# Performance work log

Hardware: AMD Instinct MI355X
Metric: run time of the kernel (lower is better)

## Reference

```python
import jax, jax.numpy as jnp
import numpy as np

ROUTING_ITERS = 3

def squash(t, axis=-1):
    sq_norm = jnp.sum(t * t, axis=axis, keepdims=True)
    scale = sq_norm / (1.0 + sq_norm)
    return scale * t / jnp.sqrt(sq_norm + 1e-8)

def setup_inputs() -> dict:
    key = jax.random.key(0)
    k1, k2 = jax.random.split(key)
    B, N, I, J, O = 64, 2048, 16, 32, 32
    x = jax.random.normal(k1, (B, N, I), dtype=jnp.float32)
    weights = jax.random.normal(k2, (N, J, O, I), dtype=jnp.float32) * 0.1
    return {"x": x, "weights": weights}

def reference(x, weights):
    B, N, _ = x.shape
    J = weights.shape[1]
    # predictions u_{j|i}: [B, N, J, O]
    predictions = jnp.einsum('bni,njoi->bnjo', x, weights)
    b = jnp.zeros((B, N, J, 1), dtype=x.dtype)
    v = None
    for i in range(ROUTING_ITERS):
        c = jax.nn.softmax(b, axis=2)                      # coupling over capsules J
        s = jnp.sum(predictions * c, axis=1, keepdims=True)  # [B,1,J,O]
        v = squash(s, axis=-1)
        if i < ROUTING_ITERS - 1:
            agreement = jnp.sum(predictions * v, axis=-1, keepdims=True)  # [B,N,J,1]
            b = b + agreement
    return jnp.squeeze(v, axis=1)  # [B, J, O]
```

## Files before the change

kernel.cpp:

```cpp
#include <hip/hip_runtime.h>
#include <hip/hip_bf16.h>

#define B_ 64
#define N_ 2048
#define I_ 16
#define J_ 32
#define O_ 32
#define JO_ 1024
#define WSPLITS 32
#define SFSPLITS 64

typedef __attribute__((ext_vector_type(8))) short bf16x8;
typedef __attribute__((ext_vector_type(16))) float f32x16;
typedef unsigned short u16;
typedef unsigned int u32;

__device__ __forceinline__ float bf2f(u16 u) {
  union { u32 i; float f; } c; c.i = ((u32)u) << 16; return c.f;
}
__device__ __forceinline__ u16 f2bf(float f) {
  union { float f; u32 i; } c; c.f = f;
  u32 r = (c.i + 0x7fffu + ((c.i >> 16) & 1u)) >> 16;
  return (u16)r;
}
__device__ __forceinline__ u32 pack2_pk(float lo, float hi) {
  u32 r;
  asm("v_cvt_pk_bf16_f32 %0, %1, %2" : "=v"(r) : "v"(lo), "v"(hi));
  return r;
}
__device__ __forceinline__ u32 scale2_pk(u32 p, float cv) {
  union { u32 i; float f; } lo, hi;
  lo.i = p << 16; hi.i = p & 0xffff0000u;
  return pack2_pk(lo.f * cv, hi.f * cv);
}
__device__ __forceinline__ float dot16(const f32x16& p, uint4 lo, uint4 hi) {
  const u32 w[8] = {lo.x, lo.y, lo.z, lo.w, hi.x, hi.y, hi.z, hi.w};
  float s = 0.f;
  #pragma unroll
  for (int k = 0; k < 8; ++k) {
    union { u32 i; float f; } a, b;
    a.i = w[k] << 16; b.i = w[k] & 0xffff0000u;
    s += p[2 * k] * a.f + p[2 * k + 1] * b.f;
  }
  return s;
}

__global__ __launch_bounds__(256) void xconv_kernel(
    const float* __restrict__ xf, u16* __restrict__ xt)
{
  const int idx = blockIdx.x * 256 + threadIdx.x;
  const int b = idx >> 11, n = idx & 2047;
  const float4* sp = (const float4*)(xf + (size_t)idx * 16);
  float4 f0 = sp[0], f1 = sp[1], f2 = sp[2], f3 = sp[3];
  uint4 d0, d1;
  d0.x = pack2_pk(f0.x, f0.y); d0.y = pack2_pk(f0.z, f0.w);
  d0.z = pack2_pk(f1.x, f1.y); d0.w = pack2_pk(f1.z, f1.w);
  d1.x = pack2_pk(f2.x, f2.y); d1.y = pack2_pk(f2.z, f2.w);
  d1.z = pack2_pk(f3.x, f3.y); d1.w = pack2_pk(f3.z, f3.w);
  uint4* dp = (uint4*)(xt + ((size_t)n * 64 + b) * 16);
  dp[0] = d0; dp[1] = d1;
}

#define WSF_NPW 16

__global__ __launch_bounds__(256, 4) void wsf_kernel(
    const float* __restrict__ wf, u16* __restrict__ wb,
    const u16* __restrict__ xt, float* __restrict__ s_part)
{
  __shared__ float red[4][2048];
  const int tid = threadIdx.x;
  const int wave = tid >> 6, lane = tid & 63;
  const int l31 = lane & 31, h = lane >> 5;
  const int j = blockIdx.x, split = blockIdx.y;
  const int n0 = (split * 4 + wave) * WSF_NPW;
  f32x16 acc0 = {0.f, 0.f, 0.f, 0.f, 0.f, 0.f, 0.f, 0.f,
                 0.f, 0.f, 0.f, 0.f, 0.f, 0.f, 0.f, 0.f};
  f32x16 acc1 = acc0;

  #pragma unroll 4
  for (int i = 0; i < WSF_NPW; ++i) {
    const int n = n0 + i;
    const size_t row = (size_t)n * JO_ + j * 32 + l31;
    const float* wsrc = wf + row * 16 + h * 8;
    const float4 f0 = *(const float4*)(wsrc);
    const float4 f1 = *(const float4*)(wsrc + 4);
    union { uint4 u4; bf16x8 bv; } wd;
    wd.u4.x = pack2_pk(f0.x, f0.y); wd.u4.y = pack2_pk(f0.z, f0.w);
    wd.u4.z = pack2_pk(f1.x, f1.y); wd.u4.w = pack2_pk(f1.z, f1.w);
    *(uint4*)(wb + row * 16 + h * 8) = wd.u4;
    const bf16x8 x0 = *(const bf16x8*)(xt + ((size_t)n * 64 + l31) * 16 + h * 8);
    const bf16x8 x1 = *(const bf16x8*)(xt + ((size_t)n * 64 + 32 + l31) * 16 + h * 8);
    acc0 = __builtin_amdgcn_mfma_f32_32x32x16_bf16(wd.bv, x0, acc0, 0, 0, 0);
    acc1 = __builtin_amdgcn_mfma_f32_32x32x16_bf16(wd.bv, x1, acc1, 0, 0, 0);
  }
  #pragma unroll
  for (int r = 0; r < 16; ++r) {
    const int o = (r & 3) + 8 * (r >> 2) + 4 * h;
    red[wave][o * 64 + l31] = acc0[r];
    red[wave][o * 64 + 32 + l31] = acc1[r];
  }
  __syncthreads();
  float* dst = s_part + (size_t)split * (JO_ * B_) + (size_t)j * 32 * 64;
  #pragma unroll
  for (int k = 0; k < 8; ++k) {
    const int idx = tid + 256 * k;
    dst[idx] = red[0][idx] + red[1][idx] + red[2][idx] + red[3][idx];
  }
}

#define SF_NPW 8

__global__ __launch_bounds__(256, 4) void sf_kernel(
    const u16* __restrict__ xt, const u16* __restrict__ wb,
    const u16* __restrict__ ct, float* __restrict__ s_part)
{
  __shared__ float red[4][2048];
  const int tid = threadIdx.x;
  const int wave = tid >> 6, lane = tid & 63;
  const int l31 = lane & 31, h = lane >> 5;
  const int j = blockIdx.x, split = blockIdx.y;
  const int n0 = (split * 4 + wave) * SF_NPW;
  f32x16 acc0 = {0.f, 0.f, 0.f, 0.f, 0.f, 0.f, 0.f, 0.f,
                 0.f, 0.f, 0.f, 0.f, 0.f, 0.f, 0.f, 0.f};
  f32x16 acc1 = acc0;

  bf16x8 wfr = *(const bf16x8*)(wb + ((size_t)n0 * JO_ + j * 32 + l31) * 16 + h * 8);
  union { bf16x8 v; u32 u[4]; } xa, xb;
  xa.v = *(const bf16x8*)(xt + ((size_t)n0 * 64 + l31) * 16 + h * 8);
  xb.v = *(const bf16x8*)(xt + ((size_t)n0 * 64 + 32 + l31) * 16 + h * 8);
  float cv0 = bf2f(ct[((size_t)j * N_ + n0) * 64 + l31]);
  float cv1 = bf2f(ct[((size_t)j * N_ + n0) * 64 + 32 + l31]);

  #pragma unroll 1
  for (int i = 0; i < SF_NPW; ++i) {
    bf16x8 wfr_n = wfr;
    union { bf16x8 v; u32 u[4]; } xa_n, xb_n;
    xa_n.v = xa.v; xb_n.v = xb.v;
    float c0n = cv0, c1n = cv1;
    if (i + 1 < SF_NPW) {
      const int n1 = n0 + i + 1;
      wfr_n = *(const bf16x8*)(wb + ((size_t)n1 * JO_ + j * 32 + l31) * 16 + h * 8);
      xa_n.v = *(const bf16x8*)(xt + ((size_t)n1 * 64 + l31) * 16 + h * 8);
      xb_n.v = *(const bf16x8*)(xt + ((size_t)n1 * 64 + 32 + l31) * 16 + h * 8);
      c0n = bf2f(ct[((size_t)j * N_ + n1) * 64 + l31]);
      c1n = bf2f(ct[((size_t)j * N_ + n1) * 64 + 32 + l31]);
    }
    union { bf16x8 v; u32 u[4]; } s0, s1;
    s0.u[0] = scale2_pk(xa.u[0], cv0); s0.u[1] = scale2_pk(xa.u[1], cv0);
    s0.u[2] = scale2_pk(xa.u[2], cv0); s0.u[3] = scale2_pk(xa.u[3], cv0);
    s1.u[0] = scale2_pk(xb.u[0], cv1); s1.u[1] = scale2_pk(xb.u[1], cv1);
    s1.u[2] = scale2_pk(xb.u[2], cv1); s1.u[3] = scale2_pk(xb.u[3], cv1);
    acc0 = __builtin_amdgcn_mfma_f32_32x32x16_bf16(wfr, s0.v, acc0, 0, 0, 0);
    acc1 = __builtin_amdgcn_mfma_f32_32x32x16_bf16(wfr, s1.v, acc1, 0, 0, 0);
    wfr = wfr_n; xa.v = xa_n.v; xb.v = xb_n.v; cv0 = c0n; cv1 = c1n;
  }
  #pragma unroll
  for (int r = 0; r < 16; ++r) {
    const int o = (r & 3) + 8 * (r >> 2) + 4 * h;
    red[wave][o * 64 + l31] = acc0[r];
    red[wave][o * 64 + 32 + l31] = acc1[r];
  }
  __syncthreads();
  float* dst = s_part + (size_t)split * (JO_ * B_) + (size_t)j * 32 * 64;
  #pragma unroll
  for (int k = 0; k < 8; ++k) {
    const int idx = tid + 256 * k;
    dst[idx] = red[0][idx] + red[1][idx] + red[2][idx] + red[3][idx];
  }
}

__global__ __launch_bounds__(256) void rs_kernel(
    const float* __restrict__ src, float* __restrict__ dst, int nsplit)
{
  const int idx = blockIdx.x * 256 + threadIdx.x;
  float s = 0.f;
  #pragma unroll 8
  for (int p = 0; p < nsplit; ++p) s += src[(size_t)p * (JO_ * B_) + idx];
  dst[idx] = s;
}

__global__ __launch_bounds__(64) void r_kernel(
    const float* __restrict__ s_red, float* __restrict__ v,
    const float* __restrict__ vprev, u16* __restrict__ v4,
    float* __restrict__ out, int mode, float scale)
{
  const int tid = threadIdx.x;
  const int jj = tid >> 5, o = tid & 31;
  const int b = blockIdx.x >> 4, jg = blockIdx.x & 15;
  const int j = jg * 2 + jj;
  const float s = s_red[(size_t)(j * 32 + o) * 64 + b] * scale;
  float sq = s * s;
  #pragma unroll
  for (int m = 16; m >= 1; m >>= 1) sq += __shfl_xor(sq, m, 64);
  const float sc = sq / (1.f + sq) * rsqrtf(sq + 1e-8f);
  const float vv = sc * s;
  const size_t off = (size_t)b * JO_ + j * 32 + o;
  const int g = o >> 3, hh = (o >> 2) & 1, rr = o & 3;
  const size_t v4off = (((size_t)j * 2 + hh) * 64 + b) * 16 + g * 4 + rr;
  if (mode == 0) { v[off] = vv; v4[v4off] = f2bf(vv); }
  else if (mode == 1) { v4[v4off] = f2bf(vv + vprev[off]); }
  else { out[off] = vv; }
}

__global__ __launch_bounds__(256, 4) void a_kernel(
    const u16* __restrict__ xt, const u16* __restrict__ wb,
    const u16* __restrict__ v4, u16* __restrict__ ct)
{
  __shared__ float lgs[64][33];
  const int tid = threadIdx.x;
  const int wave = tid >> 6, lane = tid & 63;
  const int l31 = lane & 31, h = lane >> 5;
  const int n = blockIdx.x;
  const f32x16 zero16 = {0.f, 0.f, 0.f, 0.f, 0.f, 0.f, 0.f, 0.f,
                         0.f, 0.f, 0.f, 0.f, 0.f, 0.f, 0.f, 0.f};

  const bf16x8 x0 = *(const bf16x8*)(xt + ((size_t)n * 64 + l31) * 16 + h * 8);
  const bf16x8 x1 = *(const bf16x8*)(xt + ((size_t)n * 64 + 32 + l31) * 16 + h * 8);

  {
    const int t0 = wave * 8;
    bf16x8 wfr = *(const bf16x8*)(wb + ((size_t)n * JO_ + t0 * 32 + l31) * 16 + h * 8);
    const u16* pa = v4 + (((size_t)t0 * 2 + h) * 64 + l31) * 16;
    const u16* pb = v4 + (((size_t)t0 * 2 + h) * 64 + 32 + l31) * 16;
    uint4 va0 = *(const uint4*)(pa), va1 = *(const uint4*)(pa + 8);
    uint4 vb0 = *(const uint4*)(pb), vb1 = *(const uint4*)(pb + 8);

    #pragma unroll 1
    for (int tt = 0; tt < 8; ++tt) {
      const int t = wave * 8 + tt;
      bf16x8 wfr_n = wfr;
      uint4 va0n = va0, va1n = va1, vb0n = vb0, vb1n = vb1;
      if (tt + 1 < 8) {
        const int t1 = t + 1;
        wfr_n = *(const bf16x8*)(wb + ((size_t)n * JO_ + t1 * 32 + l31) * 16 + h * 8);
        const u16* qa = v4 + (((size_t)t1 * 2 + h) * 64 + l31) * 16;
        const u16* qb = v4 + (((size_t)t1 * 2 + h) * 64 + 32 + l31) * 16;
        va0n = *(const uint4*)(qa); va1n = *(const uint4*)(qa + 8);
        vb0n = *(const uint4*)(qb); vb1n = *(const uint4*)(qb + 8);
      }
      f32x16 p0 = __builtin_amdgcn_mfma_f32_32x32x16_bf16(wfr, x0, zero16, 0, 0, 0);
      f32x16 p1 = __builtin_amdgcn_mfma_f32_32x32x16_bf16(wfr, x1, zero16, 0, 0, 0);
      float s0 = dot16(p0, va0, va1);
      float s1 = dot16(p1, vb0, vb1);
      s0 += __shfl_xor(s0, 32, 64);
      s1 += __shfl_xor(s1, 32, 64);
      lgs[lane][t] = h ? s1 : s0;
      wfr = wfr_n; va0 = va0n; va1 = va1n; vb0 = vb0n; vb1 = vb1n;
    }
  }
  __syncthreads();

  if (tid < 64) {
    const int b = tid;
    float lv[32];
    float mx = -1e30f;
    #pragma unroll
    for (int t = 0; t < 32; ++t) { lv[t] = lgs[b][t]; mx = fmaxf(mx, lv[t]); }
    float sm = 0.f;
    #pragma unroll
    for (int t = 0; t < 32; ++t) { lv[t] = __expf(lv[t] - mx); sm += lv[t]; }
    const float inv = 1.f / sm;
    #pragma unroll
    for (int t = 0; t < 32; ++t) lgs[b][t] = lv[t] * inv;
  }
  __syncthreads();

  #pragma unroll
  for (int k = 0; k < 8; ++k) {
    const int idx = k * 256 + tid;
    const int t = idx >> 6, b = idx & 63;
    ct[((size_t)t * N_ + n) * 64 + b] = f2bf(lgs[b][t]);
  }
}

extern "C" void kernel_launch(void* const* d_in, const int* in_sizes, int n_in,
                              void* d_out, int out_size, void* d_ws, size_t ws_size,
                              hipStream_t stream) {
  const float* x = (const float*)d_in[0];
  const float* w = (const float*)d_in[1];
  float* out = (float*)d_out;
  char* ws = (char*)d_ws;
  u16*   wb       = (u16*)ws;
  u16*   xt       = (u16*)(ws + (size_t)64 * 1024 * 1024);
  float* s_part32 = (float*)(ws + (size_t)68 * 1024 * 1024);
  float* s_red    = (float*)(ws + (size_t)76 * 1024 * 1024);
  float* v0       = (float*)(ws + (size_t)76 * 1024 * 1024 + 262144);
  u16*   v4       = (u16*)(ws + (size_t)76 * 1024 * 1024 + 2 * 262144);
  u16*   ct       = (u16*)(ws + (size_t)78 * 1024 * 1024);
  float* s_partSF = (float*)(ws + (size_t)88 * 1024 * 1024);

  dim3 wsfg(32, WSPLITS), wsfb(256);
  dim3 sfg(32, SFSPLITS), sfb(256);
  dim3 ag(2048), ab(256);
  dim3 rsg(256), rsb(256);
  dim3 rg(1024), rb(64);

  xconv_kernel<<<dim3(512), dim3(256), 0, stream>>>(x, xt);
  wsf_kernel<<<wsfg, wsfb, 0, stream>>>(w, wb, xt, s_part32);
  rs_kernel<<<rsg, rsb, 0, stream>>>(s_part32, s_red, WSPLITS);
  r_kernel<<<rg, rb, 0, stream>>>(s_red, v0, v0, v4, out, 0, 0.03125f);
  a_kernel<<<ag, ab, 0, stream>>>(xt, wb, v4, ct);
  sf_kernel<<<sfg, sfb, 0, stream>>>(xt, wb, ct, s_partSF);
  rs_kernel<<<rsg, rsb, 0, stream>>>(s_partSF, s_red, SFSPLITS);
  r_kernel<<<rg, rb, 0, stream>>>(s_red, v0, v0, v4, out, 1, 1.0f);
  a_kernel<<<ag, ab, 0, stream>>>(xt, wb, v4, ct);
  sf_kernel<<<sfg, sfb, 0, stream>>>(xt, wb, ct, s_partSF);
  rs_kernel<<<rsg, rsb, 0, stream>>>(s_partSF, s_red, SFSPLITS);
  r_kernel<<<rg, rb, 0, stream>>>(s_red, v0, v0, v4, out, 2, 1.0f);
}
```

Baseline: 323.2 us.

## Fuse split reduction and squash into GEMM kernels via atomics and last-block finisher

Replaces the per-split partial buffers plus separate reduce and squash kernels with atomicAdd into a single accumulator. A per-capsule counter lets the last arriving block squash and write v, v4 or the output, and then zero the accumulator for the next pass. It also halves the sf split count while doubling per-wave n work. This drops six kernel launches and the partial-sum traffic, in exchange for atomic contention, nondeterministic float summation order, and a serial tail in the finishing block.

```diff
diff --git a/kernel.cpp b/kernel.cpp
--- a/kernel.cpp
+++ b/kernel.cpp
@@ -8,7 +8,7 @@
 #define O_ 32
 #define JO_ 1024
 #define WSPLITS 32
-#define SFSPLITS 64
+#define SFSPLITS 32
 
 typedef __attribute__((ext_vector_type(8))) short bf16x8;
 typedef __attribute__((ext_vector_type(16))) float f32x16;
@@ -45,8 +45,41 @@
   return s;
 }
 
+__device__ __forceinline__ void squash_finisher(
+    float* __restrict__ s_sum, float* __restrict__ v, u16* __restrict__ v4,
+    float* __restrict__ out, int mode, float scale, int j, int tid,
+    float* fs, float* fsc)
+{
+  #pragma unroll
+  for (int k = 0; k < 8; ++k) {
+    const int idx = tid + 256 * k;
+    fs[idx] = atomicExch(&s_sum[(size_t)j * 2048 + idx], 0.0f) * scale;
+  }
+  __syncthreads();
+  if (tid < 64) {
+    float sq = 0.f;
+    #pragma unroll
+    for (int o = 0; o < 32; ++o) { const float t = fs[o * 64 + tid]; sq += t * t; }
+    fsc[tid] = sq / (1.f + sq) * rsqrtf(sq + 1e-8f);
+  }
+  __syncthreads();
+  #pragma unroll
+  for (int k = 0; k < 8; ++k) {
+    const int idx = tid + 256 * k;
+    const int o = idx >> 6, b = idx & 63;
+    const float vv = fs[idx] * fsc[b];
+    const int g = o >> 3, hh = (o >> 2) & 1, rr = o & 3;
+    const size_t v4off = (((size_t)j * 2 + hh) * 64 + b) * 16 + g * 4 + rr;
+    const size_t off = (size_t)b * JO_ + j * 32 + o;
+    if (mode == 0)      { v[off] = vv; v4[v4off] = f2bf(vv); }
+    else if (mode == 1) { v4[v4off] = f2bf(vv + v[off]); }
+    else                { out[off] = vv; }
+  }
+}
+
 __global__ __launch_bounds__(256) void xconv_kernel(
-    const float* __restrict__ xf, u16* __restrict__ xt)
+    const float* __restrict__ xf, u16* __restrict__ xt,
+    float* __restrict__ s_sum, u32* __restrict__ cnt)
 {
   const int idx = blockIdx.x * 256 + threadIdx.x;
   const int b = idx >> 11, n = idx & 2047;
@@ -59,15 +92,20 @@
   d1.z = pack2_pk(f3.x, f3.y); d1.w = pack2_pk(f3.z, f3.w);
   uint4* dp = (uint4*)(xt + ((size_t)n * 64 + b) * 16);
   dp[0] = d0; dp[1] = d1;
+  if (idx < JO_ * B_) s_sum[idx] = 0.f;
+  if (idx < 96) cnt[idx] = 0;
 }
 
 #define WSF_NPW 16
 
 __global__ __launch_bounds__(256, 4) void wsf_kernel(
     const float* __restrict__ wf, u16* __restrict__ wb,
-    const u16* __restrict__ xt, float* __restrict__ s_part)
+    const u16* __restrict__ xt, float* __restrict__ s_sum,
+    u32* __restrict__ cnt, float* __restrict__ v, u16* __restrict__ v4,
+    float* __restrict__ out)
 {
   __shared__ float red[4][2048];
+  __shared__ u32 isLast;
   const int tid = threadIdx.x;
   const int wave = tid >> 6, lane = tid & 63;
   const int l31 = lane & 31, h = lane >> 5;
@@ -100,21 +138,32 @@
     red[wave][o * 64 + 32 + l31] = acc1[r];
   }
   __syncthreads();
-  float* dst = s_part + (size_t)split * (JO_ * B_) + (size_t)j * 32 * 64;
   #pragma unroll
   for (int k = 0; k < 8; ++k) {
     const int idx = tid + 256 * k;
-    dst[idx] = red[0][idx] + red[1][idx] + red[2][idx] + red[3][idx];
-  }
-}
-
-#define SF_NPW 8
+    const float sum = red[0][idx] + red[1][idx] + red[2][idx] + red[3][idx];
+    atomicAdd(&s_sum[(size_t)j * 2048 + idx], sum);
+  }
+  __syncthreads();
+  if (tid == 0) {
+    __threadfence();
+    isLast = (atomicAdd(&cnt[j], 1u) == WSPLITS - 1);
+  }
+  __syncthreads();
+  if (isLast)
+    squash_finisher(s_sum, v, v4, out, 0, 0.03125f, j, tid, red[0], red[1]);
+}
+
+#define SF_NPW 16
 
 __global__ __launch_bounds__(256, 4) void sf_kernel(
     const u16* __restrict__ xt, const u16* __restrict__ wb,
-    const u16* __restrict__ ct, float* __restrict__ s_part)
+    const u16* __restrict__ ct, float* __restrict__ s_sum,
+    u32* __restrict__ cnt, float* __restrict__ v, u16* __restrict__ v4,
+    float* __restrict__ out, int mode)
 {
   __shared__ float red[4][2048];
+  __shared__ u32 isLast;
   const int tid = threadIdx.x;
   const int wave = tid >> 6, lane = tid & 63;
   const int l31 = lane & 31, h = lane >> 5;
@@ -125,34 +174,34 @@
   f32x16 acc1 = acc0;
 
   bf16x8 wfr = *(const bf16x8*)(wb + ((size_t)n0 * JO_ + j * 32 + l31) * 16 + h * 8);
-  union { bf16x8 v; u32 u[4]; } xa, xb;
-  xa.v = *(const bf16x8*)(xt + ((size_t)n0 * 64 + l31) * 16 + h * 8);
-  xb.v = *(const bf16x8*)(xt + ((size_t)n0 * 64 + 32 + l31) * 16 + h * 8);
+  union { bf16x8 v_; u32 u[4]; } xa, xb;
+  xa.v_ = *(const bf16x8*)(xt + ((size_t)n0 * 64 + l31) * 16 + h * 8);
+  xb.v_ = *(const bf16x8*)(xt + ((size_t)n0 * 64 + 32 + l31) * 16 + h * 8);
   float cv0 = bf2f(ct[((size_t)j * N_ + n0) * 64 + l31]);
   float cv1 = bf2f(ct[((size_t)j * N_ + n0) * 64 + 32 + l31]);
 
   #pragma unroll 1
   for (int i = 0; i < SF_NPW; ++i) {
     bf16x8 wfr_n = wfr;
-    union { bf16x8 v; u32 u[4]; } xa_n, xb_n;
-    xa_n.v = xa.v; xb_n.v = xb.v;
+    union { bf16x8 v_; u32 u[4]; } xa_n, xb_n;
+    xa_n.v_ = xa.v_; xb_n.v_ = xb.v_;
     float c0n = cv0, c1n = cv1;
     if (i + 1 < SF_NPW) {
       const int n1 = n0 + i + 1;
       wfr_n = *(const bf16x8*)(wb + ((size_t)n1 * JO_ + j * 32 + l31) * 16 + h * 8);
-      xa_n.v = *(const bf16x8*)(xt + ((size_t)n1 * 64 + l31) * 16 + h * 8);
-      xb_n.v = *(const bf16x8*)(xt + ((size_t)n1 * 64 + 32 + l31) * 16 + h * 8);
+      xa_n.v_ = *(const bf16x8*)(xt + ((size_t)n1 * 64 + l31) * 16 + h * 8);
+      xb_n.v_ = *(const bf16x8*)(xt + ((size_t)n1 * 64 + 32 + l31) * 16 + h * 8);
       c0n = bf2f(ct[((size_t)j * N_ + n1) * 64 + l31]);
       c1n = bf2f(ct[((size_t)j * N_ + n1) * 64 + 32 + l31]);
     }
-    union { bf16x8 v; u32 u[4]; } s0, s1;
+    union { bf16x8 v_; u32 u[4]; } s0, s1;
     s0.u[0] = scale2_pk(xa.u[0], cv0); s0.u[1] = scale2_pk(xa.u[1], cv0);
     s0.u[2] = scale2_pk(xa.u[2], cv0); s0.u[3] = scale2_pk(xa.u[3], cv0);
     s1.u[0] = scale2_pk(xb.u[0], cv1); s1.u[1] = scale2_pk(xb.u[1], cv1);
     s1.u[2] = scale2_pk(xb.u[2], cv1); s1.u[3] = scale2_pk(xb.u[3], cv1);
-    acc0 = __builtin_amdgcn_mfma_f32_32x32x16_bf16(wfr, s0.v, acc0, 0, 0, 0);
-    acc1 = __builtin_amdgcn_mfma_f32_32x32x16_bf16(wfr, s1.v, acc1, 0, 0, 0);
-    wfr = wfr_n; xa.v = xa_n.v; xb.v = xb_n.v; cv0 = c0n; cv1 = c1n;
+    acc0 = __builtin_amdgcn_mfma_f32_32x32x16_bf16(wfr, s0.v_, acc0, 0, 0, 0);
+    acc1 = __builtin_amdgcn_mfma_f32_32x32x16_bf16(wfr, s1.v_, acc1, 0, 0, 0);
+    wfr = wfr_n; xa.v_ = xa_n.v_; xb.v_ = xb_n.v_; cv0 = c0n; cv1 = c1n;
   }
   #pragma unroll
   for (int r = 0; r < 16; ++r) {
@@ -161,45 +210,20 @@
     red[wave][o * 64 + 32 + l31] = acc1[r];
   }
   __syncthreads();
-  float* dst = s_part + (size_t)split * (JO_ * B_) + (size_t)j * 32 * 64;
   #pragma unroll
   for (int k = 0; k < 8; ++k) {
     const int idx = tid + 256 * k;
-    dst[idx] = red[0][idx] + red[1][idx] + red[2][idx] + red[3][idx];
-  }
-}
-
-__global__ __launch_bounds__(256) void rs_kernel(
-    const float* __restrict__ src, float* __restrict__ dst, int nsplit)
-{
-  const int idx = blockIdx.x * 256 + threadIdx.x;
-  float s = 0.f;
-  #pragma unroll 8
-  for (int p = 0; p < nsplit; ++p) s += src[(size_t)p * (JO_ * B_) + idx];
-  dst[idx] = s;
-}
-
-__global__ __launch_bounds__(64) void r_kernel(
-    const float* __restrict__ s_red, float* __restrict__ v,
-    const float* __restrict__ vprev, u16* __restrict__ v4,
-    float* __restrict__ out, int mode, float scale)
-{
-  const int tid = threadIdx.x;
-  const int jj = tid >> 5, o = tid & 31;
-  const int b = blockIdx.x >> 4, jg = blockIdx.x & 15;
-  const int j = jg * 2 + jj;
-  const float s = s_red[(size_t)(j * 32 + o) * 64 + b] * scale;
-  float sq = s * s;
-  #pragma unroll
-  for (int m = 16; m >= 1; m >>= 1) sq += __shfl_xor(sq, m, 64);
-  const float sc = sq / (1.f + sq) * rsqrtf(sq + 1e-8f);
-  const float vv = sc * s;
-  const size_t off = (size_t)b * JO_ + j * 32 + o;
-  const int g = o >> 3, hh = (o >> 2) & 1, rr = o & 3;
-  const size_t v4off = (((size_t)j * 2 + hh) * 64 + b) * 16 + g * 4 + rr;
-  if (mode == 0) { v[off] = vv; v4[v4off] = f2bf(vv); }
-  else if (mode == 1) { v4[v4off] = f2bf(vv + vprev[off]); }
-  else { out[off] = vv; }
+    const float sum = red[0][idx] + red[1][idx] + red[2][idx] + red[3][idx];
+    atomicAdd(&s_sum[(size_t)j * 2048 + idx], sum);
+  }
+  __syncthreads();
+  if (tid == 0) {
+    __threadfence();
+    isLast = (atomicAdd(&cnt[j], 1u) == SFSPLITS - 1);
+  }
+  __syncthreads();
+  if (isLast)
+    squash_finisher(s_sum, v, v4, out, mode, 1.0f, j, tid, red[0], red[1]);
 }
 
 __global__ __launch_bounds__(256, 4) void a_kernel(
@@ -280,31 +304,21 @@
   const float* w = (const float*)d_in[1];
   float* out = (float*)d_out;
   char* ws = (char*)d_ws;
-  u16*   wb       = (u16*)ws;
-  u16*   xt       = (u16*)(ws + (size_t)64 * 1024 * 1024);
-  float* s_part32 = (float*)(ws + (size_t)68 * 1024 * 1024);
-  float* s_red    = (float*)(ws + (size_t)76 * 1024 * 1024);
-  float* v0       = (float*)(ws + (size_t)76 * 1024 * 1024 + 262144);
-  u16*   v4       = (u16*)(ws + (size_t)76 * 1024 * 1024 + 2 * 262144);
-  u16*   ct       = (u16*)(ws + (size_t)78 * 1024 * 1024);
-  float* s_partSF = (float*)(ws + (size_t)88 * 1024 * 1024);
-
-  dim3 wsfg(32, WSPLITS), wsfb(256);
-  dim3 sfg(32, SFSPLITS), sfb(256);
-  dim3 ag(2048), ab(256);
-  dim3 rsg(256), rsb(256);
-  dim3 rg(1024), rb(64);
-
-  xconv_kernel<<<dim3(512), dim3(256), 0, stream>>>(x, xt);
-  wsf_kernel<<<wsfg, wsfb, 0, stream>>>(w, wb, xt, s_part32);
-  rs_kernel<<<rsg, rsb, 0, stream>>>(s_part32, s_red, WSPLITS);
-  r_kernel<<<rg, rb, 0, stream>>>(s_red, v0, v0, v4, out, 0, 0.03125f);
-  a_kernel<<<ag, ab, 0, stream>>>(xt, wb, v4, ct);
-  sf_kernel<<<sfg, sfb, 0, stream>>>(xt, wb, ct, s_partSF);
-  rs_kernel<<<rsg, rsb, 0, stream>>>(s_partSF, s_red, SFSPLITS);
-  r_kernel<<<rg, rb, 0, stream>>>(s_red, v0, v0, v4, out, 1, 1.0f);
-  a_kernel<<<ag, ab, 0, stream>>>(xt, wb, v4, ct);
-  sf_kernel<<<sfg, sfb, 0, stream>>>(xt, wb, ct, s_partSF);
-  rs_kernel<<<rsg, rsb, 0, stream>>>(s_partSF, s_red, SFSPLITS);
-  r_kernel<<<rg, rb, 0, stream>>>(s_red, v0, v0, v4, out, 2, 1.0f);
-}
+  u16*   wb    = (u16*)ws;
+  u16*   xt    = (u16*)(ws + (size_t)64 * 1024 * 1024);
+  float* s_sum = (float*)(ws + (size_t)68 * 1024 * 1024);
+  float* v0    = (float*)(ws + (size_t)68 * 1024 * 1024 + 262144);
+  u16*   v4    = (u16*)(ws + (size_t)68 * 1024 * 1024 + 2 * 262144);
+  u32*   cnt   = (u32*)(ws + (size_t)68 * 1024 * 1024 + 2 * 262144 + 131072);
+  u16*   ct    = (u16*)(ws + (size_t)70 * 1024 * 1024);
+
+  dim3 wsfg(32, WSPLITS), sfg(32, SFSPLITS), b256(256);
+  dim3 ag(2048);
+
+  xconv_kernel<<<dim3(512), b256, 0, stream>>>(x, xt, s_sum, cnt);
+  wsf_kernel<<<wsfg, b256, 0, stream>>>(w, wb, xt, s_sum, cnt, v0, v4, out);
+  a_kernel<<<ag, b256, 0, stream>>>(xt, wb, v4, ct);
+  sf_kernel<<<sfg, b256, 0, stream>>>(xt, wb, ct, s_sum, cnt + 32, v0, v4, out, 1);
+  a_kernel<<<ag, b256, 0, stream>>>(xt, wb, v4, ct);
+  sf_kernel<<<sfg, b256, 0, stream>>>(xt, wb, ct, s_sum, cnt + 64, v0, v4, out, 2);
+}
```

New measurement: 409.5 us. 26.7% more time.
